# Performance work log

Measured on AMD Instinct MI355X. Metric: run time of the kernel, lower is better.

The kernel has to match this reference:

```python
import jax, jax.numpy as jnp
import numpy as np
import math

T_MAX = 1000.0  # init kwarg T_max


def setup_inputs() -> dict:
    key = jax.random.key(0)
    ks = jax.random.split(key, 9)
    B, L, C, M, E = 32, 1024, 2, 96, 1024
    return {
        "x": jax.random.normal(ks[0], (B, L, C), dtype=jnp.float32),
        "t": jax.random.uniform(ks[1], (B, L, C), dtype=jnp.float32) * T_MAX,
        "mask": jax.random.uniform(ks[2], (B, L, C), dtype=jnp.float32),
        "W_emb": jax.random.normal(ks[3], (1, E), dtype=jnp.float32),  # Linear(1, E) weight (input_dim=1)
        "b_emb": jax.random.normal(ks[4], (E,), dtype=jnp.float32),
        "alpha_sin": jax.random.normal(ks[5], (C, M, E), dtype=jnp.float32),
        "alpha_cos": jax.random.normal(ks[6], (C, M, E), dtype=jnp.float32),
        "beta_sin": jax.random.normal(ks[7], (C, M, E), dtype=jnp.float32),
        "beta_cos": jax.random.normal(ks[8], (C, M, E), dtype=jnp.float32),
    }


def reference(x, t, mask, W_emb, b_emb, alpha_sin, alpha_cos, beta_sin, beta_cos):
    # x, t, mask: [B, L, C]; alpha_*/beta_*: [C, M, E]
    B, L, C = x.shape
    M, E = alpha_sin.shape[1], alpha_sin.shape[2]

    ar = jnp.arange(M, dtype=x.dtype)                      # Fourier frequencies 0..M-1
    phase = (2.0 * math.pi / T_MAX) * t[..., None] * ar     # [B, L, C, M]
    s, c = jnp.sin(phase), jnp.cos(phase)

    # to_emb: Linear(1, E) applied to each channel scalar -> [B, L, C, E]
    emb = x[..., None] * W_emb[0] + b_emb

    # per-channel time modulation: alpha = sin@A_s + cos@A_c, beta likewise
    alpha = (jnp.einsum('blcm,cme->blce', s, alpha_sin)
             + jnp.einsum('blcm,cme->blce', c, alpha_cos))
    beta = (jnp.einsum('blcm,cme->blce', s, beta_sin)
            + jnp.einsum('blcm,cme->blce', c, beta_cos))
    mod = emb * alpha + beta                                # [B, L, C, E]

    # torch.cat over channel blocks along dim 1 -> [B, C*L, E]
    mod_flat = mod.transpose(0, 2, 1, 3).reshape(B, C * L, E)
    t_flat = t.transpose(0, 2, 1).reshape(B, C * L, 1)
    mask_flat = mask.transpose(0, 2, 1).reshape(B, C * L, 1)

    # argsort by time and gather-reorder
    idx = jnp.argsort(t_flat, axis=1)                       # [B, C*L, 1]
    out_x = jnp.take_along_axis(mod_flat, jnp.broadcast_to(idx, mod_flat.shape), axis=1)
    out_t = jnp.take_along_axis(t_flat, idx, axis=1)
    out_m = jnp.take_along_axis(mask_flat, idx, axis=1)
    return out_x, out_t, out_m
```

## Files before the change

kernel.cpp:

```cpp
#include <hip/hip_runtime.h>
#include <hip/hip_bf16.h>

#define B_  32
#define L_  1024
#define C_  2
#define M_  96
#define E_  1024
#define K_  192
#define NROWS (B_*C_*L_)

typedef __attribute__((ext_vector_type(8))) short short8;
typedef __attribute__((ext_vector_type(4))) float f32x4;

static __device__ __forceinline__ unsigned short f2bf(float f) {
    unsigned u = __float_as_uint(f);
    u += 0x7fff + ((u >> 16) & 1);
    return (unsigned short)(u >> 16);
}

__global__ void pack_tables(const float* __restrict__ as, const float* __restrict__ ac,
                            const float* __restrict__ bs, const float* __restrict__ bc,
                            unsigned short* __restrict__ pT) {
    int tid = blockIdx.x * blockDim.x + threadIdx.x;
    if (tid >= 2*2*6*4*1024) return;
    int e    = tid & 1023;
    int kc   = (tid >> 10) & 3;
    int rest = tid >> 12;
    int ks   = rest % 6;
    int t2c  = rest / 6;
    int tab2 = t2c >> 1, ch = t2c & 1;
    const float* ssrc = tab2 ? bs : as;
    const float* csrc = tab2 ? bc : ac;
    short8 v;
#pragma unroll
    for (int j = 0; j < 8; ++j) {
        int k = ks*32 + kc*8 + j;
        float f = (k < M_) ? ssrc[((size_t)ch*M_ + k)*E_ + e]
                           : csrc[((size_t)ch*M_ + (k - M_))*E_ + e];
        v[j] = (short)f2bf(f);
    }
    *(short8*)&pT[(size_t)tid * 8] = v;
}

__global__ void sprep(const float* __restrict__ t, unsigned short* __restrict__ S) {
    int tid = blockIdx.x * blockDim.x + threadIdx.x;
    if (tid >= NROWS*24) return;
    int q   = tid % 24;
    int row = tid / 24;
    int b = row >> 11, ch = (row >> 10) & 1, l = row & 1023;
    float tv = t[((size_t)b*L_ + l)*C_ + ch];
    const float w = 6.2831853071795864769f / 1000.0f;
    float wt = w * tv;
    ushort4 sv, cv;
#pragma unroll
    for (int j = 0; j < 4; ++j) {
        int m = q*4 + j;
        float s, c;
        sincosf(wt * (float)m, &s, &c);
        ((unsigned short*)&sv)[j] = f2bf(s);
        ((unsigned short*)&cv)[j] = f2bf(c);
    }
    *(ushort4*)&S[(size_t)row*K_ + q*4]       = sv;
    *(ushort4*)&S[(size_t)row*K_ + M_ + q*4]  = cv;
}

__global__ __launch_bounds__(1024) void sort_kernel(
        const float* __restrict__ t, const float* __restrict__ mask,
        float* __restrict__ out_t, float* __restrict__ out_m,
        int* __restrict__ inv) {
    __shared__ unsigned long long sk[2048];
    int b = blockIdx.x, tid = threadIdx.x;
    for (int i = tid; i < 2048; i += 1024) {
        int ch = i >> 10, l = i & 1023;
        float tv = t[((size_t)b*L_ + l)*C_ + ch];
        sk[i] = ((unsigned long long)__float_as_uint(tv) << 32) | (unsigned)i;
    }
    __syncthreads();
    for (int k = 2; k <= 2048; k <<= 1) {
        for (int j = k >> 1; j > 0; j >>= 1) {
            int i = ((tid & ~(j - 1)) << 1) | (tid & (j - 1));
            int p = i | j;
            bool up = ((i & k) == 0);
            unsigned long long a = sk[i], c = sk[p];
            if ((a > c) == up) { sk[i] = c; sk[p] = a; }
            __syncthreads();
        }
    }
    for (int i = tid; i < 2048; i += 1024) {
        unsigned long long key = sk[i];
        unsigned src = (unsigned)(key & 0xffffffffu);
        out_t[(size_t)b*2048 + i] = __uint_as_float((unsigned)(key >> 32));
        int ch = (int)(src >> 10), l = (int)(src & 1023);
        out_m[(size_t)b*2048 + i] = mask[((size_t)b*L_ + l)*C_ + ch];
        inv[b*2048 + (int)src] = i;
    }
}

__global__ __launch_bounds__(256) void main_kernel(
        const unsigned short* __restrict__ S, const unsigned short* __restrict__ pT,
        const int* __restrict__ inv, const float* __restrict__ x,
        const float* __restrict__ W, const float* __restrict__ bemb,
        float* __restrict__ out_x) {
    int lane = threadIdx.x & 63;
    int wave = threadIdx.x >> 6;
    int lr = lane & 15, lk = lane >> 4;
    int rowbase = blockIdx.x * 64;
    int b  = rowbase >> 11;
    int ch = (rowbase >> 10) & 1;
    int n0 = blockIdx.y * 256 + wave * 64;

    const unsigned short* pA = pT + (size_t)ch       * (6*4*1024*8);
    const unsigned short* pB = pT + (size_t)(2 + ch) * (6*4*1024*8);

    f32x4 accA[4][4] = {};
    f32x4 accB[4][4] = {};

#pragma unroll
    for (int ks = 0; ks < 6; ++ks) {
        short8 a[4];
#pragma unroll
        for (int rt = 0; rt < 4; ++rt) {
            int row = rowbase + rt*16 + lr;
            a[rt] = *(const short8*)&S[(size_t)row*K_ + ks*32 + lk*8];
        }
#pragma unroll
        for (int nt = 0; nt < 4; ++nt) {
            int n = n0 + nt*16 + lr;
            size_t off = (((size_t)ks*4 + lk)*1024 + n)*8;
            short8 bA = *(const short8*)&pA[off];
            short8 bB = *(const short8*)&pB[off];
#pragma unroll
            for (int rt = 0; rt < 4; ++rt) {
                accA[rt][nt] = __builtin_amdgcn_mfma_f32_16x16x32_bf16(a[rt], bA, accA[rt][nt], 0, 0, 0);
                accB[rt][nt] = __builtin_amdgcn_mfma_f32_16x16x32_bf16(a[rt], bB, accB[rt][nt], 0, 0, 0);
            }
        }
    }

    float wv[4], bv[4];
#pragma unroll
    for (int nt = 0; nt < 4; ++nt) {
        int e = n0 + nt*16 + lr;
        wv[nt] = W[e];
        bv[nt] = bemb[e];
    }
    int l_base = rowbase & 1023;
#pragma unroll
    for (int rt = 0; rt < 4; ++rt) {
#pragma unroll
        for (int r = 0; r < 4; ++r) {
            int l = l_base + rt*16 + lk*4 + r;
            float xv = x[((size_t)b*L_ + l)*C_ + ch];
            int dst = inv[(b*C_ + ch)*L_ + l];
            float* orow = out_x + ((size_t)b*2048 + dst)*E_;
#pragma unroll
            for (int nt = 0; nt < 4; ++nt) {
                float emb = xv*wv[nt] + bv[nt];
                orow[n0 + nt*16 + lr] = emb*accA[rt][nt][r] + accB[rt][nt][r];
            }
        }
    }
}

extern "C" void kernel_launch(void* const* d_in, const int* in_sizes, int n_in,
                              void* d_out, int out_size, void* d_ws, size_t ws_size,
                              hipStream_t stream) {
    const float* x    = (const float*)d_in[0];
    const float* t    = (const float*)d_in[1];
    const float* mask = (const float*)d_in[2];
    const float* W    = (const float*)d_in[3];
    const float* bemb = (const float*)d_in[4];
    const float* as_  = (const float*)d_in[5];
    const float* ac_  = (const float*)d_in[6];
    const float* bs_  = (const float*)d_in[7];
    const float* bc_  = (const float*)d_in[8];

    float* out_x = (float*)d_out;
    float* out_t = out_x + (size_t)B_*2048*E_;
    float* out_m = out_t + (size_t)B_*2048;

    char* ws = (char*)d_ws;
    int*            inv = (int*)ws;
    unsigned short* pT  = (unsigned short*)(ws + 262144);
    unsigned short* S   = (unsigned short*)(ws + 262144 + 1572864);

    pack_tables<<<dim3(384), dim3(256), 0, stream>>>(as_, ac_, bs_, bc_, pT);
    sprep<<<dim3((NROWS*24)/256), dim3(256), 0, stream>>>(t, S);
    sort_kernel<<<dim3(B_), dim3(1024), 0, stream>>>(t, mask, out_t, out_m, inv);
    main_kernel<<<dim3(NROWS/64, E_/256), dim3(256), 0, stream>>>(S, pT, inv, x, W, bemb, out_x);
}
```

Measured before the change: 383.4 us.

## Fuse sin/cos feature generation into main GEMM kernel via LDS

Removes the separate sprep kernel and its global S buffer. Each block now builds its 64 rows of bf16 sin/cos features in shared memory, using a sincos angle-addition recurrence instead of one sincosf per frequency. x and inv are staged in LDS, and each block loops over all four 256-wide E chunks so the features are computed once per row. The cost is a 4x smaller grid, more serial work per block, and small accuracy drift from the recurrence.

```diff
diff --git a/kernel.cpp b/kernel.cpp
--- a/kernel.cpp
+++ b/kernel.cpp
@@ -42,28 +42,6 @@
     *(short8*)&pT[(size_t)tid * 8] = v;
 }
 
-__global__ void sprep(const float* __restrict__ t, unsigned short* __restrict__ S) {
-    int tid = blockIdx.x * blockDim.x + threadIdx.x;
-    if (tid >= NROWS*24) return;
-    int q   = tid % 24;
-    int row = tid / 24;
-    int b = row >> 11, ch = (row >> 10) & 1, l = row & 1023;
-    float tv = t[((size_t)b*L_ + l)*C_ + ch];
-    const float w = 6.2831853071795864769f / 1000.0f;
-    float wt = w * tv;
-    ushort4 sv, cv;
-#pragma unroll
-    for (int j = 0; j < 4; ++j) {
-        int m = q*4 + j;
-        float s, c;
-        sincosf(wt * (float)m, &s, &c);
-        ((unsigned short*)&sv)[j] = f2bf(s);
-        ((unsigned short*)&cv)[j] = f2bf(c);
-    }
-    *(ushort4*)&S[(size_t)row*K_ + q*4]       = sv;
-    *(ushort4*)&S[(size_t)row*K_ + M_ + q*4]  = cv;
-}
-
 __global__ __launch_bounds__(1024) void sort_kernel(
         const float* __restrict__ t, const float* __restrict__ mask,
         float* __restrict__ out_t, float* __restrict__ out_m,
@@ -97,66 +75,105 @@
 }
 
 __global__ __launch_bounds__(256) void main_kernel(
-        const unsigned short* __restrict__ S, const unsigned short* __restrict__ pT,
-        const int* __restrict__ inv, const float* __restrict__ x,
+        const unsigned short* __restrict__ pT, const int* __restrict__ inv,
+        const float* __restrict__ x, const float* __restrict__ t,
         const float* __restrict__ W, const float* __restrict__ bemb,
         float* __restrict__ out_x) {
-    int lane = threadIdx.x & 63;
-    int wave = threadIdx.x >> 6;
+    __shared__ unsigned short S_lds[64 * 200];
+    __shared__ float x_s[64];
+    __shared__ int   inv_s[64];
+
+    int tid  = threadIdx.x;
+    int lane = tid & 63;
+    int wave = tid >> 6;
     int lr = lane & 15, lk = lane >> 4;
     int rowbase = blockIdx.x * 64;
     int b  = rowbase >> 11;
     int ch = (rowbase >> 10) & 1;
-    int n0 = blockIdx.y * 256 + wave * 64;
+    int l_base = rowbase & 1023;
+
+    {
+        int row = tid >> 2;
+        int q   = tid & 3;
+        int l   = l_base + row;
+        float tv = t[((size_t)b*L_ + l)*C_ + ch];
+        const float w = 6.2831853071795864769f / 1000.0f;
+        float wt = w * tv;
+        float s1, c1; sincosf(wt, &s1, &c1);
+        float sm, cm; sincosf(wt * (float)(q*24), &sm, &cm);
+        unsigned short* rowp = &S_lds[row * 200];
+#pragma unroll
+        for (int jj = 0; jj < 6; ++jj) {
+            ushort4 sv, cv;
+#pragma unroll
+            for (int j = 0; j < 4; ++j) {
+                ((unsigned short*)&sv)[j] = f2bf(sm);
+                ((unsigned short*)&cv)[j] = f2bf(cm);
+                float ns = sm*c1 + cm*s1;
+                float nc = cm*c1 - sm*s1;
+                sm = ns; cm = nc;
+            }
+            *(ushort4*)&rowp[q*24 + jj*4]      = sv;
+            *(ushort4*)&rowp[96 + q*24 + jj*4] = cv;
+        }
+        if (tid < 64) {
+            int ll = l_base + tid;
+            x_s[tid]   = x[((size_t)b*L_ + ll)*C_ + ch];
+            inv_s[tid] = inv[(b*C_ + ch)*L_ + ll];
+        }
+    }
+    __syncthreads();
 
     const unsigned short* pA = pT + (size_t)ch       * (6*4*1024*8);
     const unsigned short* pB = pT + (size_t)(2 + ch) * (6*4*1024*8);
 
-    f32x4 accA[4][4] = {};
-    f32x4 accB[4][4] = {};
-
-#pragma unroll
-    for (int ks = 0; ks < 6; ++ks) {
-        short8 a[4];
+#pragma unroll 1
+    for (int cq = 0; cq < 4; ++cq) {
+        int n0 = cq*256 + wave*64;
+        f32x4 accA[4][4] = {};
+        f32x4 accB[4][4] = {};
+#pragma unroll
+        for (int ks = 0; ks < 6; ++ks) {
+            short8 a[4];
+#pragma unroll
+            for (int rt = 0; rt < 4; ++rt) {
+                int rl = rt*16 + lr;
+                a[rt] = *(const short8*)&S_lds[rl*200 + ks*32 + lk*8];
+            }
+#pragma unroll
+            for (int nt = 0; nt < 4; ++nt) {
+                int n = n0 + nt*16 + lr;
+                size_t off = (((size_t)ks*4 + lk)*1024 + n)*8;
+                short8 bA = *(const short8*)&pA[off];
+                short8 bB = *(const short8*)&pB[off];
+#pragma unroll
+                for (int rt = 0; rt < 4; ++rt) {
+                    accA[rt][nt] = __builtin_amdgcn_mfma_f32_16x16x32_bf16(a[rt], bA, accA[rt][nt], 0, 0, 0);
+                    accB[rt][nt] = __builtin_amdgcn_mfma_f32_16x16x32_bf16(a[rt], bB, accB[rt][nt], 0, 0, 0);
+                }
+            }
+        }
+
+        float wv[4], bv[4];
+#pragma unroll
+        for (int nt = 0; nt < 4; ++nt) {
+            int e = n0 + nt*16 + lr;
+            wv[nt] = W[e];
+            bv[nt] = bemb[e];
+        }
 #pragma unroll
         for (int rt = 0; rt < 4; ++rt) {
-            int row = rowbase + rt*16 + lr;
-            a[rt] = *(const short8*)&S[(size_t)row*K_ + ks*32 + lk*8];
-        }
-#pragma unroll
-        for (int nt = 0; nt < 4; ++nt) {
-            int n = n0 + nt*16 + lr;
-            size_t off = (((size_t)ks*4 + lk)*1024 + n)*8;
-            short8 bA = *(const short8*)&pA[off];
-            short8 bB = *(const short8*)&pB[off];
-#pragma unroll
-            for (int rt = 0; rt < 4; ++rt) {
-                accA[rt][nt] = __builtin_amdgcn_mfma_f32_16x16x32_bf16(a[rt], bA, accA[rt][nt], 0, 0, 0);
-                accB[rt][nt] = __builtin_amdgcn_mfma_f32_16x16x32_bf16(a[rt], bB, accB[rt][nt], 0, 0, 0);
-            }
-        }
-    }
-
-    float wv[4], bv[4];
-#pragma unroll
-    for (int nt = 0; nt < 4; ++nt) {
-        int e = n0 + nt*16 + lr;
-        wv[nt] = W[e];
-        bv[nt] = bemb[e];
-    }
-    int l_base = rowbase & 1023;
-#pragma unroll
-    for (int rt = 0; rt < 4; ++rt) {
-#pragma unroll
-        for (int r = 0; r < 4; ++r) {
-            int l = l_base + rt*16 + lk*4 + r;
-            float xv = x[((size_t)b*L_ + l)*C_ + ch];
-            int dst = inv[(b*C_ + ch)*L_ + l];
-            float* orow = out_x + ((size_t)b*2048 + dst)*E_;
-#pragma unroll
-            for (int nt = 0; nt < 4; ++nt) {
-                float emb = xv*wv[nt] + bv[nt];
-                orow[n0 + nt*16 + lr] = emb*accA[rt][nt][r] + accB[rt][nt][r];
+#pragma unroll
+            for (int r = 0; r < 4; ++r) {
+                int row_l = rt*16 + lk*4 + r;
+                float xv = x_s[row_l];
+                int dst  = inv_s[row_l];
+                float* orow = out_x + ((size_t)b*2048 + dst)*E_;
+#pragma unroll
+                for (int nt = 0; nt < 4; ++nt) {
+                    float emb = xv*wv[nt] + bv[nt];
+                    orow[n0 + nt*16 + lr] = emb*accA[rt][nt][r] + accB[rt][nt][r];
+                }
             }
         }
     }
@@ -182,10 +199,8 @@
     char* ws = (char*)d_ws;
     int*            inv = (int*)ws;
     unsigned short* pT  = (unsigned short*)(ws + 262144);
-    unsigned short* S   = (unsigned short*)(ws + 262144 + 1572864);
 
     pack_tables<<<dim3(384), dim3(256), 0, stream>>>(as_, ac_, bs_, bc_, pT);
-    sprep<<<dim3((NROWS*24)/256), dim3(256), 0, stream>>>(t, S);
     sort_kernel<<<dim3(B_), dim3(1024), 0, stream>>>(t, mask, out_t, out_m, inv);
-    main_kernel<<<dim3(NROWS/64, E_/256), dim3(256), 0, stream>>>(S, pT, inv, x, W, bemb, out_x);
-}
+    main_kernel<<<dim3(NROWS/64), dim3(256), 0, stream>>>(pT, inv, x, t, W, bemb, out_x);
+}
```

After: 375.9 us. No clear change (-1.9%).
